# Performance work log

Measured on AMD Instinct MI355X. Metric: run time of the kernel, lower is better.

The kernel has to match this reference:

```python
import jax, jax.numpy as jnp
import numpy as np

N = 40000       # nodes
E = 640000      # edges (before self-loops)
D_IN = 128      # input_dim
D = 128         # hidden_dim
HEADS = 8
C = D // HEADS  # per-head channels = 16
L = 3           # num_layers
G = 64          # number of graphs for mean pool
SLOPE = 0.2     # GATConv leaky_relu negative slope
EPS_LN = 1e-5


def setup_inputs() -> dict:
    key = jax.random.key(0)
    ks = jax.random.split(key, 12)
    x = jax.random.normal(ks[0], (N, D_IN), dtype=jnp.float32)
    edge_index = jax.random.randint(ks[1], (2, E), 0, N, dtype=jnp.int32)
    batch = jnp.sort(jax.random.randint(ks[2], (N,), 0, G, dtype=jnp.int32))
    s = 0.05
    return {
        "x": x,
        "edge_index": edge_index,
        "batch": batch,
        "W_in": jax.random.normal(ks[3], (D_IN, D), dtype=jnp.float32) * s,
        "b_in": jnp.zeros((D,), dtype=jnp.float32),
        "W_l": jax.random.normal(ks[4], (L, D, D), dtype=jnp.float32) * s,
        "att_src": jax.random.normal(ks[5], (L, HEADS, C), dtype=jnp.float32) * s,
        "att_dst": jax.random.normal(ks[6], (L, HEADS, C), dtype=jnp.float32) * s,
        "bias_l": jnp.zeros((L, D), dtype=jnp.float32),
        "gamma": jnp.ones((L, D), dtype=jnp.float32),
        "beta": jnp.zeros((L, D), dtype=jnp.float32),
    }


def _gat_layer(x, src, dst, W, a_s, a_d, b):
    n = x.shape[0]
    h = (x @ W).reshape(n, HEADS, C)            # [N,H,C]
    al_src = jnp.sum(h * a_s, axis=-1)          # [N,H]
    al_dst = jnp.sum(h * a_d, axis=-1)          # [N,H]
    logits = jax.nn.leaky_relu(al_src[src] + al_dst[dst], SLOPE)  # [Et,H]
    # segment softmax over incoming edges of each dst node
    m = jax.ops.segment_max(logits, dst, num_segments=n)
    m = jnp.where(jnp.isfinite(m), m, 0.0)
    e = jnp.exp(logits - m[dst])
    denom = jax.ops.segment_sum(e, dst, num_segments=n)
    alpha = e / (denom[dst] + 1e-16)            # [Et,H]
    msg = h[src] * alpha[:, :, None]            # [Et,H,C]
    out = jax.ops.segment_sum(msg, dst, num_segments=n)  # [N,H,C]
    return out.reshape(n, HEADS * C) + b


def _layer_norm(x, g, b):
    mu = jnp.mean(x, axis=-1, keepdims=True)
    var = jnp.var(x, axis=-1, keepdims=True)
    return (x - mu) * jax.lax.rsqrt(var + EPS_LN) * g + b


def reference(x, edge_index, batch, W_in, b_in, W_l, att_src, att_dst, bias_l, gamma, beta):
    n = x.shape[0]
    x = x @ W_in + b_in
    # add self loops (PyG GATConv default)
    loops = jnp.arange(n, dtype=edge_index.dtype)
    src = jnp.concatenate([edge_index[0], loops])
    dst = jnp.concatenate([edge_index[1], loops])
    for l in range(L):
        x = x + _gat_layer(x, src, dst, W_l[l], att_src[l], att_dst[l], bias_l[l])
        x = _layer_norm(x, gamma[l], beta[l])
        x = jax.nn.relu(x)
    # global mean pool over graph segments
    cnt = jax.ops.segment_sum(jnp.ones((n,), x.dtype), batch, num_segments=G)
    s = jax.ops.segment_sum(x, batch, num_segments=G)
    return s / jnp.maximum(cnt, 1.0)[:, None]
```

## Files before the change

kernel.cpp:

```cpp
#include <hip/hip_runtime.h>
#include <hip/hip_bf16.h>
#include <math.h>

#define NN 40000
#define DD 128
#define HH 8
#define EE 640000
#define ET (EE + NN)
#define GG 64
#define SLOPE 0.2f
#define CAP 64

typedef unsigned int uint;
typedef unsigned short ushort;
typedef _Float16 f16x8 __attribute__((ext_vector_type(8)));
typedef __attribute__((ext_vector_type(4))) float f32x4;

__device__ inline ushort f2h(float f) {
    union { ushort s; _Float16 h; } c;
    c.h = (_Float16)f;
    return c.s;
}
__device__ inline float h_lo(uint u) {
    union { ushort s; _Float16 h; } c;
    c.s = (ushort)(u & 0xffffu);
    return (float)c.h;
}
__device__ inline float h_hi(uint u) {
    union { ushort s; _Float16 h; } c;
    c.s = (ushort)(u >> 16);
    return (float)c.h;
}

__global__ void prep_wt(const float* __restrict__ Win, const float* __restrict__ Wl,
                        ushort* __restrict__ wt) {
    int i = blockIdx.x * 256 + threadIdx.x;
    if (i >= 4 * 128 * 128) return;
    int w = i >> 14, rem = i & 16383, n = rem >> 7, k = rem & 127;
    const float* src = (w == 0) ? Win : (Wl + (size_t)(w - 1) * 16384);
    wt[i] = f2h(src[k * 128 + n]);
}

__global__ void fill_pad(const int* __restrict__ ei,
                         int* __restrict__ deg, int* __restrict__ colp) {
    int e = blockIdx.x * blockDim.x + threadIdx.x;
    if (e >= ET) return;
    int s, d;
    if (e < EE) { s = ei[e]; d = ei[EE + e]; } else { s = d = e - EE; }
    int pos = atomicAdd(&deg[d], 1);
    if (pos < CAP) colp[(d << 6) + pos] = s;
}

__global__ __launch_bounds__(256) void gemm_mfma(const ushort* __restrict__ A16,
                                                 const float* __restrict__ Afp,
                                                 const ushort* __restrict__ WT,
                                                 const float* __restrict__ bias,
                                                 const float* __restrict__ atts,
                                                 const float* __restrict__ attd,
                                                 float* __restrict__ xout,
                                                 ushort* __restrict__ x16out,
                                                 float* __restrict__ al_s,
                                                 float* __restrict__ al_d,
                                                 ushort* __restrict__ h16out) {
    __shared__ ushort lds[128 * 136];
    int t = threadIdx.x;
    int wv = t >> 6, l = t & 63;
    int row0 = blockIdx.x * 64;

    {
        const uint4* src = (const uint4*)WT;
        for (int i = t; i < 2048; i += 256) {
            int r = i >> 4, c = i & 15;
            *(uint4*)((uint*)(lds + r * 136) + c * 4) = src[i];
        }
    }
    __syncthreads();

    int q = l >> 4, r16 = l & 15;
    f16x8 a0, a1, a2, a3;
    if (Afp) {
        const float* ar = Afp + (size_t)(row0 + wv * 16 + r16) * 128 + q * 8;
        {
            float4 fa = *(const float4*)(ar);
            float4 fb = *(const float4*)(ar + 4);
            a0 = (f16x8){(_Float16)fa.x, (_Float16)fa.y, (_Float16)fa.z, (_Float16)fa.w,
                         (_Float16)fb.x, (_Float16)fb.y, (_Float16)fb.z, (_Float16)fb.w};
        }
        {
            float4 fa = *(const float4*)(ar + 32);
            float4 fb = *(const float4*)(ar + 36);
            a1 = (f16x8){(_Float16)fa.x, (_Float16)fa.y, (_Float16)fa.z, (_Float16)fa.w,
                         (_Float16)fb.x, (_Float16)fb.y, (_Float16)fb.z, (_Float16)fb.w};
        }
        {
            float4 fa = *(const float4*)(ar + 64);
            float4 fb = *(const float4*)(ar + 68);
            a2 = (f16x8){(_Float16)fa.x, (_Float16)fa.y, (_Float16)fa.z, (_Float16)fa.w,
                         (_Float16)fb.x, (_Float16)fb.y, (_Float16)fb.z, (_Float16)fb.w};
        }
        {
            float4 fa = *(const float4*)(ar + 96);
            float4 fb = *(const float4*)(ar + 100);
            a3 = (f16x8){(_Float16)fa.x, (_Float16)fa.y, (_Float16)fa.z, (_Float16)fa.w,
                         (_Float16)fb.x, (_Float16)fb.y, (_Float16)fb.z, (_Float16)fb.w};
        }
    } else {
        const ushort* arow = A16 + (size_t)(row0 + wv * 16 + r16) * 128 + q * 8;
        a0 = *(const f16x8*)(arow);
        a1 = *(const f16x8*)(arow + 32);
        a2 = *(const f16x8*)(arow + 64);
        a3 = *(const f16x8*)(arow + 96);
    }
    f32x4 acc[8];
    #pragma unroll
    for (int c = 0; c < 8; ++c) acc[c] = (f32x4){0.f, 0.f, 0.f, 0.f};
    #pragma unroll
    for (int c = 0; c < 8; ++c) {
        const ushort* bp = lds + (c * 16 + r16) * 136 + q * 8;
        f16x8 b0 = *(const f16x8*)(bp);
        f16x8 b1 = *(const f16x8*)(bp + 32);
        f16x8 b2 = *(const f16x8*)(bp + 64);
        f16x8 b3 = *(const f16x8*)(bp + 96);
        acc[c] = __builtin_amdgcn_mfma_f32_16x16x32_f16(a0, b0, acc[c], 0, 0, 0);
        acc[c] = __builtin_amdgcn_mfma_f32_16x16x32_f16(a1, b1, acc[c], 0, 0, 0);
        acc[c] = __builtin_amdgcn_mfma_f32_16x16x32_f16(a2, b2, acc[c], 0, 0, 0);
        acc[c] = __builtin_amdgcn_mfma_f32_16x16x32_f16(a3, b3, acc[c], 0, 0, 0);
    }
    __syncthreads();

    float* tile = (float*)lds + wv * (16 * 132);
    #pragma unroll
    for (int c = 0; c < 8; ++c)
        #pragma unroll
        for (int i = 0; i < 4; ++i)
            tile[(q * 4 + i) * 132 + c * 16 + r16] = acc[c][i];
    __asm__ volatile("s_waitcnt lgkmcnt(0)" ::: "memory");

    #pragma unroll
    for (int uu = 0; uu < 2; ++uu) {
        int u = l + uu * 64;
        int row = u & 15, head = u >> 4;
        int n = row0 + wv * 16 + row;
        const float* rp = tile + row * 132 + head * 16;
        float4 h0 = *(const float4*)(rp);
        float4 h1 = *(const float4*)(rp + 4);
        float4 h2 = *(const float4*)(rp + 8);
        float4 h3 = *(const float4*)(rp + 12);
        if (h16out) {
            const float4* as4 = (const float4*)(atts + head * 16);
            const float4* ad4 = (const float4*)(attd + head * 16);
            float ss = 0.f, sd = 0.f;
            float4 a, b;
            a = as4[0]; b = ad4[0];
            ss += h0.x*a.x + h0.y*a.y + h0.z*a.z + h0.w*a.w;
            sd += h0.x*b.x + h0.y*b.y + h0.z*b.z + h0.w*b.w;
            a = as4[1]; b = ad4[1];
            ss += h1.x*a.x + h1.y*a.y + h1.z*a.z + h1.w*a.w;
            sd += h1.x*b.x + h1.y*b.y + h1.z*b.z + h1.w*b.w;
            a = as4[2]; b = ad4[2];
            ss += h2.x*a.x + h2.y*a.y + h2.z*a.z + h2.w*a.w;
            sd += h2.x*b.x + h2.y*b.y + h2.z*b.z + h2.w*b.w;
            a = as4[3]; b = ad4[3];
            ss += h3.x*a.x + h3.y*a.y + h3.z*a.z + h3.w*a.w;
            sd += h3.x*b.x + h3.y*b.y + h3.z*b.z + h3.w*b.w;
            al_s[(size_t)n * 8 + head] = ss;
            al_d[(size_t)n * 8 + head] = sd;
            uint4 p0, p1;
            p0.x = (uint)f2h(h0.x) | ((uint)f2h(h0.y) << 16);
            p0.y = (uint)f2h(h0.z) | ((uint)f2h(h0.w) << 16);
            p0.z = (uint)f2h(h1.x) | ((uint)f2h(h1.y) << 16);
            p0.w = (uint)f2h(h1.z) | ((uint)f2h(h1.w) << 16);
            p1.x = (uint)f2h(h2.x) | ((uint)f2h(h2.y) << 16);
            p1.y = (uint)f2h(h2.z) | ((uint)f2h(h2.w) << 16);
            p1.z = (uint)f2h(h3.x) | ((uint)f2h(h3.y) << 16);
            p1.w = (uint)f2h(h3.z) | ((uint)f2h(h3.w) << 16);
            uint4* dst = (uint4*)((uint*)h16out + (size_t)n * 64 + head * 8);
            dst[0] = p0; dst[1] = p1;
        } else {
            const float4* b4 = (const float4*)(bias + head * 16);
            float4 bb;
            bb = b4[0]; h0.x += bb.x; h0.y += bb.y; h0.z += bb.z; h0.w += bb.w;
            bb = b4[1]; h1.x += bb.x; h1.y += bb.y; h1.z += bb.z; h1.w += bb.w;
            bb = b4[2]; h2.x += bb.x; h2.y += bb.y; h2.z += bb.z; h2.w += bb.w;
            bb = b4[3]; h3.x += bb.x; h3.y += bb.y; h3.z += bb.z; h3.w += bb.w;
            float4* xo = (float4*)(xout + (size_t)n * 128 + head * 16);
            xo[0] = h0; xo[1] = h1; xo[2] = h2; xo[3] = h3;
            uint4 p0, p1;
            p0.x = (uint)f2h(h0.x) | ((uint)f2h(h0.y) << 16);
            p0.y = (uint)f2h(h0.z) | ((uint)f2h(h0.w) << 16);
            p0.z = (uint)f2h(h1.x) | ((uint)f2h(h1.y) << 16);
            p0.w = (uint)f2h(h1.z) | ((uint)f2h(h1.w) << 16);
            p1.x = (uint)f2h(h2.x) | ((uint)f2h(h2.y) << 16);
            p1.y = (uint)f2h(h2.z) | ((uint)f2h(h2.w) << 16);
            p1.z = (uint)f2h(h3.x) | ((uint)f2h(h3.y) << 16);
            p1.w = (uint)f2h(h3.z) | ((uint)f2h(h3.w) << 16);
            uint4* dst = (uint4*)((uint*)x16out + (size_t)n * 64 + head * 8);
            dst[0] = p0; dst[1] = p1;
        }
    }
}

__global__ __launch_bounds__(256) void gat_fused(const int* __restrict__ deg_a,
                                                 const int* __restrict__ colp,
                                                 const float* __restrict__ al_s,
                                                 const float* __restrict__ al_d,
                                                 const uint* __restrict__ h16,
                                                 const float* __restrict__ bias,
                                                 const float* __restrict__ gamma,
                                                 const float* __restrict__ beta,
                                                 float* __restrict__ x,
                                                 uint* __restrict__ x16u) {
    __shared__ float accv[4][128];
    int wv = threadIdx.x >> 6;
    int wave = blockIdx.x * 4 + wv;
    int lane = threadIdx.x & 63;
    if (wave >= NN) return;
    const int d = wave;
    const int deg = min(deg_a[d], CAP);

    const int gg = lane >> 4;
    const int cc = lane & 15;
    const int hd2 = cc >> 1;
    int col_r = 0;
    if (lane < deg) col_r = colp[(d << 6) + lane];
    const float ald = al_d[(size_t)d * 8 + hd2];

    float ac[8] = {0.f, 0.f, 0.f, 0.f, 0.f, 0.f, 0.f, 0.f};
    float dsum = 0.f;
    for (int j = gg; j < deg; j += 4) {
        int s = __shfl(col_r, j);
        float tt = al_s[(size_t)s * 8 + hd2] + ald;
        tt = tt >= 0.f ? tt : SLOPE * tt;
        float e = __expf(tt);
        dsum += e;
        uint4 hv = *((const uint4*)(h16 + ((size_t)s << 6)) + cc);
        ac[0] += e * h_lo(hv.x); ac[1] += e * h_hi(hv.x);
        ac[2] += e * h_lo(hv.y); ac[3] += e * h_hi(hv.y);
        ac[4] += e * h_lo(hv.z); ac[5] += e * h_hi(hv.z);
        ac[6] += e * h_lo(hv.w); ac[7] += e * h_hi(hv.w);
    }
    #pragma unroll
    for (int i = 0; i < 8; ++i) {
        ac[i] += __shfl_xor(ac[i], 16);
        ac[i] += __shfl_xor(ac[i], 32);
    }
    dsum += __shfl_xor(dsum, 16);
    dsum += __shfl_xor(dsum, 32);
    float r = 1.f / (dsum + 1e-16f);
    if (gg == 0) {
        #pragma unroll
        for (int i2 = 0; i2 < 4; ++i2)
            *(float2*)&accv[wv][(cc << 3) + (i2 << 1)] =
                make_float2(ac[2 * i2] * r, ac[2 * i2 + 1] * r);
    }

    __asm__ volatile("s_waitcnt lgkmcnt(0)" ::: "memory");
    int colA = lane << 1;
    float2 av = *(const float2*)&accv[wv][colA];
    size_t base = (size_t)d * 128;
    float2 xv = *(const float2*)(x + base + colA);
    float2 bv = *(const float2*)(bias + colA);
    float v0 = xv.x + av.x + bv.x;
    float v1 = xv.y + av.y + bv.y;
    float sum = v0 + v1;
    #pragma unroll
    for (int off = 32; off; off >>= 1) sum += __shfl_xor(sum, off);
    float mu = sum * (1.f / 128.f);
    float d0 = v0 - mu, d1 = v1 - mu;
    float var = d0 * d0 + d1 * d1;
    #pragma unroll
    for (int off = 32; off; off >>= 1) var += __shfl_xor(var, off);
    float inv = rsqrtf(var * (1.f / 128.f) + 1e-5f);
    float2 gv = *(const float2*)(gamma + colA);
    float2 btv = *(const float2*)(beta + colA);
    float o0 = fmaxf((d0 * inv) * gv.x + btv.x, 0.f);
    float o1 = fmaxf((d1 * inv) * gv.y + btv.y, 0.f);
    *(float2*)(x + base + colA) = make_float2(o0, o1);
    if (x16u) x16u[(size_t)d * 64 + lane] = (uint)f2h(o0) | ((uint)f2h(o1) << 16);
}

__global__ __launch_bounds__(256) void pool_kernel(const float* __restrict__ x,
                                                   const int* __restrict__ batch,
                                                   float* __restrict__ s,
                                                   float* __restrict__ cnt) {
    __shared__ float acc[8][8][128];
    __shared__ float accc[8][8];
    const int NPB = 64;
    int t = threadIdx.x;
    int g = t >> 5;
    int lane = t & 31;
    int n0 = blockIdx.x * NPB;
    int nend = min(n0 + NPB, NN);
    int b0 = batch[n0];
    int span = batch[nend - 1] - b0 + 1;
    for (int i = t; i < 8 * 8 * 128; i += 256) ((float*)acc)[i] = 0.f;
    if (t < 64) ((float*)accc)[t] = 0.f;
    __syncthreads();
    if (span <= 8) {
        float4 r = make_float4(0.f, 0.f, 0.f, 0.f);
        float rc = 0.f;
        int cb = -1;
        for (int n = n0 + g; n < nend; n += 8) {
            int b = batch[n] - b0;
            if (b != cb) {
                if (cb >= 0) {
                    float4* p = (float4*)&acc[g][cb][lane * 4];
                    float4 cu = *p;
                    cu.x += r.x; cu.y += r.y; cu.z += r.z; cu.w += r.w;
                    *p = cu;
                    if (lane == 0) accc[g][cb] += rc;
                }
                r = make_float4(0.f, 0.f, 0.f, 0.f); rc = 0.f; cb = b;
            }
            float4 v = *(const float4*)(x + (size_t)n * 128 + lane * 4);
            r.x += v.x; r.y += v.y; r.z += v.z; r.w += v.w;
            rc += 1.f;
        }
        if (cb >= 0) {
            float4* p = (float4*)&acc[g][cb][lane * 4];
            float4 cu = *p;
            cu.x += r.x; cu.y += r.y; cu.z += r.z; cu.w += r.w;
            *p = cu;
            if (lane == 0) accc[g][cb] += rc;
        }
        __syncthreads();
        for (int i = t; i < span * 128; i += 256) {
            int b = i >> 7, c = i & 127;
            float v = 0.f;
            #pragma unroll
            for (int gq = 0; gq < 8; ++gq) v += acc[gq][b][c];
            atomicAdd(&s[(size_t)(b0 + b) * 128 + c], v);
        }
        if (t < span) {
            float v = 0.f;
            #pragma unroll
            for (int gq = 0; gq < 8; ++gq) v += accc[gq][t];
            atomicAdd(&cnt[b0 + t], v);
        }
    } else {
        int colc = t & 127, grp = t >> 7;
        for (int n = n0 + grp; n < nend; n += 2) {
            int b = batch[n];
            atomicAdd(&s[(size_t)b * 128 + colc], x[(size_t)n * 128 + colc]);
            if (colc == 0) atomicAdd(&cnt[b], 1.f);
        }
    }
}

__global__ void finalize_out(const float* __restrict__ s,
                             const float* __restrict__ cnt,
                             float* __restrict__ out) {
    int i = blockIdx.x * blockDim.x + threadIdx.x;
    if (i < GG * DD) out[i] = s[i] / fmaxf(cnt[i >> 7], 1.f);
}

extern "C" void kernel_launch(void* const* d_in, const int* in_sizes, int n_in,
                              void* d_out, int out_size, void* d_ws, size_t ws_size,
                              hipStream_t stream) {
    const float* x_in   = (const float*)d_in[0];
    const int*   ei     = (const int*)d_in[1];
    const int*   batch  = (const int*)d_in[2];
    const float* W_in   = (const float*)d_in[3];
    const float* b_in   = (const float*)d_in[4];
    const float* W_l    = (const float*)d_in[5];
    const float* att_s  = (const float*)d_in[6];
    const float* att_d  = (const float*)d_in[7];
    const float* bias_l = (const float*)d_in[8];
    const float* gamma  = (const float*)d_in[9];
    const float* beta   = (const float*)d_in[10];
    float* out = (float*)d_out;

    float* ws    = (float*)d_ws;
    float* xbuf  = ws;
    float* al_s  = xbuf + (size_t)NN * DD;
    float* al_d  = al_s + (size_t)NN * HH;
    float* pool  = al_d + (size_t)NN * HH;
    float* cnt   = pool + (size_t)GG * DD;
    int*   deg   = (int*)(cnt + GG);
    int*   colp  = deg + NN;
    ushort* x16  = (ushort*)(colp + (size_t)NN * CAP);
    ushort* h16  = x16 + (size_t)NN * 128;
    ushort* wt   = h16 + (size_t)NN * 128;

    hipMemsetAsync(deg, 0, NN * sizeof(int), stream);
    fill_pad<<<(ET + 255) / 256, 256, 0, stream>>>(ei, deg, colp);

    prep_wt<<<256, 256, 0, stream>>>(W_in, W_l, wt);

    gemm_mfma<<<625, 256, 0, stream>>>(nullptr, x_in, wt, b_in, nullptr, nullptr,
                                       xbuf, x16, nullptr, nullptr, nullptr);

    for (int l = 0; l < 3; ++l) {
        gemm_mfma<<<625, 256, 0, stream>>>(x16, nullptr, wt + (size_t)(1 + l) * 16384, nullptr,
                                           att_s + l * 128, att_d + l * 128,
                                           nullptr, nullptr, al_s, al_d, h16);
        gat_fused<<<NN / 4, 256, 0, stream>>>(deg, colp, al_s, al_d, (const uint*)h16,
                                              bias_l + l * 128, gamma + l * 128, beta + l * 128,
                                              xbuf, (l < 2) ? (uint*)x16 : nullptr);
    }

    hipMemsetAsync(pool, 0, (size_t)(GG * DD + GG) * sizeof(float), stream);
    pool_kernel<<<NN / 64, 256, 0, stream>>>(xbuf, batch, pool, cnt);
    finalize_out<<<(GG * DD + 255) / 256, 256, 0, stream>>>(pool, cnt, out);
}
```

Measured before the change: 222.7 us.

## Build padded adjacency via two-pass bucket binning with shared-memory row assembly

Result: faster. 207.3 us (-6.9%).

```diff
diff --git a/kernel.cpp b/kernel.cpp
--- a/kernel.cpp
+++ b/kernel.cpp
@@ -10,6 +10,9 @@
 #define GG 64
 #define SLOPE 0.2f
 #define CAP 64
+#define NBKT 157
+#define CAPB 6144
+#define EPT 16
 
 typedef unsigned int uint;
 typedef unsigned short ushort;
@@ -30,6 +33,14 @@
     union { ushort s; _Float16 h; } c;
     c.s = (ushort)(u >> 16);
     return (float)c.h;
+}
+
+__global__ void zero_ws(int* __restrict__ gcnt, float* __restrict__ pool,
+                        float* __restrict__ cnt) {
+    int i = blockIdx.x * 256 + threadIdx.x;
+    if (i < NBKT) gcnt[i] = 0;
+    if (i < GG * DD) pool[i] = 0.f;
+    if (i < GG) cnt[i] = 0.f;
 }
 
 __global__ void prep_wt(const float* __restrict__ Win, const float* __restrict__ Wl,
@@ -41,14 +52,69 @@
     wt[i] = f2h(src[k * 128 + n]);
 }
 
-__global__ void fill_pad(const int* __restrict__ ei,
-                         int* __restrict__ deg, int* __restrict__ colp) {
-    int e = blockIdx.x * blockDim.x + threadIdx.x;
-    if (e >= ET) return;
-    int s, d;
-    if (e < EE) { s = ei[e]; d = ei[EE + e]; } else { s = d = e - EE; }
-    int pos = atomicAdd(&deg[d], 1);
-    if (pos < CAP) colp[(d << 6) + pos] = s;
+__global__ __launch_bounds__(256) void bin_edges(const int* __restrict__ ei,
+                                                 int* __restrict__ gcnt,
+                                                 uint* __restrict__ bucket) {
+    __shared__ int hist[NBKT];
+    __shared__ int base[NBKT];
+    int tid = threadIdx.x;
+    int e0 = blockIdx.x * (256 * EPT);
+    for (int j = tid; j < NBKT; j += 256) hist[j] = 0;
+    __syncthreads();
+
+    int la[EPT];
+    #pragma unroll
+    for (int i = 0; i < EPT; ++i) {
+        int e = e0 + tid + i * 256;
+        la[i] = -1;
+        if (e < ET) {
+            int d = (e < EE) ? ei[EE + e] : (e - EE);
+            la[i] = atomicAdd(&hist[d >> 8], 1);
+        }
+    }
+    __syncthreads();
+    for (int j = tid; j < NBKT; j += 256) base[j] = atomicAdd(&gcnt[j], hist[j]);
+    __syncthreads();
+
+    #pragma unroll
+    for (int i = 0; i < EPT; ++i) {
+        int e = e0 + tid + i * 256;
+        if (e < ET) {
+            int s, d;
+            if (e < EE) { s = ei[e]; d = ei[EE + e]; } else { s = d = e - EE; }
+            int b = d >> 8;
+            int pos = base[b] + la[i];
+            if (pos < CAPB) bucket[b * CAPB + pos] = (uint)s | ((uint)(d & 255) << 16);
+        }
+    }
+}
+
+__global__ __launch_bounds__(256) void build_rows(const uint* __restrict__ bucket,
+                                                  const int* __restrict__ gcnt,
+                                                  ushort* __restrict__ colp,
+                                                  int* __restrict__ deg) {
+    __shared__ ushort cols[256 * 64];
+    __shared__ int ldeg[256];
+    int tid = threadIdx.x;
+    int b = blockIdx.x;
+    ldeg[tid] = 0;
+    __syncthreads();
+    int cnt = min(gcnt[b], CAPB);
+    for (int i = tid; i < cnt; i += 256) {
+        uint e = bucket[b * CAPB + i];
+        int dl = e >> 16;
+        int p = atomicAdd(&ldeg[dl], 1);
+        if (p < CAP) cols[(dl << 6) + p] = (ushort)(e & 0xffffu);
+    }
+    __syncthreads();
+    const uint4* src = (const uint4*)cols;
+    for (int i = tid; i < 2048; i += 256) {
+        int row = i >> 3;
+        int n = (b << 8) + row;
+        if (n < NN) ((uint4*)colp)[(size_t)n * 8 + (i & 7)] = src[i];
+    }
+    int n = (b << 8) + tid;
+    if (n < NN) deg[n] = min(ldeg[tid], CAP);
 }
 
 __global__ __launch_bounds__(256) void gemm_mfma(const ushort* __restrict__ A16,
@@ -201,7 +267,7 @@
 }
 
 __global__ __launch_bounds__(256) void gat_fused(const int* __restrict__ deg_a,
-                                                 const int* __restrict__ colp,
+                                                 const ushort* __restrict__ colp,
                                                  const float* __restrict__ al_s,
                                                  const float* __restrict__ al_d,
                                                  const uint* __restrict__ h16,
@@ -216,13 +282,13 @@
     int lane = threadIdx.x & 63;
     if (wave >= NN) return;
     const int d = wave;
-    const int deg = min(deg_a[d], CAP);
+    const int deg = deg_a[d];
 
     const int gg = lane >> 4;
     const int cc = lane & 15;
     const int hd2 = cc >> 1;
     int col_r = 0;
-    if (lane < deg) col_r = colp[(d << 6) + lane];
+    if (lane < deg) col_r = (int)colp[((size_t)d << 6) + lane];
     const float ald = al_d[(size_t)d * 8 + hd2];
 
     float ac[8] = {0.f, 0.f, 0.f, 0.f, 0.f, 0.f, 0.f, 0.f};
@@ -376,14 +442,17 @@
     float* al_d  = al_s + (size_t)NN * HH;
     float* pool  = al_d + (size_t)NN * HH;
     float* cnt   = pool + (size_t)GG * DD;
-    int*   deg   = (int*)(cnt + GG);
-    int*   colp  = deg + NN;
-    ushort* x16  = (ushort*)(colp + (size_t)NN * CAP);
+    int*   gcnt  = (int*)(cnt + GG);
+    int*   deg   = gcnt + 160;
+    uint*  bucket = (uint*)(deg + NN);
+    ushort* colp = (ushort*)(bucket + (size_t)NBKT * CAPB);
+    ushort* x16  = colp + (size_t)NN * CAP;
     ushort* h16  = x16 + (size_t)NN * 128;
     ushort* wt   = h16 + (size_t)NN * 128;
 
-    hipMemsetAsync(deg, 0, NN * sizeof(int), stream);
-    fill_pad<<<(ET + 255) / 256, 256, 0, stream>>>(ei, deg, colp);
+    zero_ws<<<(GG * DD + 255) / 256, 256, 0, stream>>>(gcnt, pool, cnt);
+    bin_edges<<<(ET + 256 * EPT - 1) / (256 * EPT), 256, 0, stream>>>(ei, gcnt, bucket);
+    build_rows<<<NBKT, 256, 0, stream>>>(bucket, gcnt, colp, deg);
 
     prep_wt<<<256, 256, 0, stream>>>(W_in, W_l, wt);
 
@@ -399,7 +468,6 @@
                                               xbuf, (l < 2) ? (uint*)x16 : nullptr);
     }
 
-    hipMemsetAsync(pool, 0, (size_t)(GG * DD + GG) * sizeof(float), stream);
     pool_kernel<<<NN / 64, 256, 0, stream>>>(xbuf, batch, pool, cnt);
     finalize_out<<<(GG * DD + 255) / 256, 256, 0, stream>>>(pool, cnt, out);
 }
```
